# Kernel tuning notes

Hardware: AMD Instinct MI355X
Metric: run time of the kernel (lower is better)

## Reference

```python
import jax, jax.numpy as jnp
import numpy as np
import math

B, TQ, TK, D = 4, 1024, 1024, 1024
H, DK, DV = 16, 64, 64


def _ln(x, g, b, eps=1e-5):
    m = x.mean(-1, keepdims=True)
    v = ((x - m) ** 2).mean(-1, keepdims=True)
    return (x - m) * jax.lax.rsqrt(v + eps) * g + b


def setup_inputs() -> dict:
    key = jax.random.key(0)
    ks = jax.random.split(key, 24)
    s = 0.02
    inp = {
        "x": jax.random.normal(ks[0], (B, TQ, D), jnp.float32),
        "y": jax.random.normal(ks[1], (B, TK, D), jnp.float32),
        "mask": jax.random.randint(ks[2], (B, TK), 0, 2).astype(bool),
        # pre-attention layernorms (affine)
        "ln1_g": jnp.ones((D,)), "ln1_b": jnp.zeros((D,)),
        "ln2_g": jnp.ones((D,)), "ln2_b": jnp.zeros((D,)),
        # mha1 projections
        "q_w": jax.random.normal(ks[3], (D, H * DK)) * s, "q_b": jnp.zeros((H * DK,)),
        "k_w": jax.random.normal(ks[4], (D, H * DK)) * s, "k_b": jnp.zeros((H * DK,)),
        "v_w": jax.random.normal(ks[5], (D, H * DV)) * s, "v_b": jnp.zeros((H * DV,)),
        "o_w": jax.random.normal(ks[6], (H * DV, D)) * s, "o_b": jnp.zeros((D,)),
        # MLP: [LN, ReLU, Linear] x 2 over sizes [D, D, D]
        "mln1_g": jnp.ones((D,)), "mln1_b": jnp.zeros((D,)),
        "l1_w": jax.random.normal(ks[7], (D, D)) * s, "l1_b": jnp.zeros((D,)),
        "mln2_g": jnp.ones((D,)), "mln2_b": jnp.zeros((D,)),
        "l2_w": jax.random.normal(ks[8], (D, D)) * s, "l2_b": jnp.zeros((D,)),
    }
    return inp


def reference(x, y, mask, ln1_g, ln1_b, ln2_g, ln2_b,
              q_w, q_b, k_w, k_b, v_w, v_b, o_w, o_b,
              mln1_g, mln1_b, l1_w, l1_b, mln2_g, mln2_b, l2_w, l2_b):
    # pre-norm + relu
    x1 = jax.nn.relu(_ln(x, ln1_g, ln1_b))
    y1 = jax.nn.relu(_ln(y, ln2_g, ln2_b))
    # cross attention (mha1)
    b, t, _ = x1.shape
    q = (x1 @ q_w + q_b).reshape(b, t, H, DK)
    k = (y1 @ k_w + k_b).reshape(b, -1, H, DK)
    v = (y1 @ v_w + v_b).reshape(b, -1, H, DV)
    logits = jnp.einsum('bthd,bThd->bhtT', q, k) * (1.0 / math.sqrt(DK))
    logits = jnp.where(mask[:, None, None, :], logits, -1e30)
    w = jax.nn.softmax(logits, axis=-1)
    attn = jnp.einsum('bhtT,bThd->bthd', w, v).reshape(b, t, H * DV)
    x = x + (attn @ o_w + o_b)
    # MLP: LN -> ReLU -> Linear, twice
    h = jax.nn.relu(_ln(x, mln1_g, mln1_b)) @ l1_w + l1_b
    out = jax.nn.relu(_ln(h, mln2_g, mln2_b)) @ l2_w + l2_b
    return out
```

## Files before the change

kernel.cpp:

```cpp
#include <hip/hip_runtime.h>
#include <hip/hip_bf16.h>
#include <math.h>

#define D_MODEL 1024
#define NTOK    4096

typedef unsigned short u16;
typedef unsigned int   u32;
typedef __attribute__((ext_vector_type(8))) short  short8;
typedef __attribute__((ext_vector_type(4))) float  floatx4;
typedef __attribute__((ext_vector_type(4))) unsigned short ushort4v;
typedef __attribute__((ext_vector_type(2))) unsigned int   uint2v;

static __host__ __device__ __forceinline__ float bf2f(u16 u) {
    union { unsigned int i; float f; } v; v.i = ((unsigned int)u) << 16; return v.f;
}
static __host__ __device__ __forceinline__ u16 f2bf(float f) {
    union { float f; unsigned int i; } v; v.f = f;
    unsigned int r = (v.i + 0x7FFFu + ((v.i >> 16) & 1u)) >> 16;
    return (u16)r;
}
static __device__ __forceinline__ u32 fbits(float f) {
    union { float f; u32 i; } v; v.f = f; return v.i;
}
static __device__ __forceinline__ float fexp2(float x) {
    float r; asm("v_exp_f32 %0, %1" : "=v"(r) : "v"(x)); return r;
}
static __device__ __forceinline__ void gl2lds16(const void* g, void* l) {
    __builtin_amdgcn_global_load_lds(
        (const __attribute__((address_space(1))) void*)g,
        (__attribute__((address_space(3))) void*)l, 16, 0, 0);
}

__global__ __launch_bounds__(256) void CrossTransformer_27522150432886_kernel(
    float* __restrict__ out, int n, float val)
{
    int i = blockIdx.x * 256 + threadIdx.x;
    if (i < n) out[i] = val;
}

__global__ __launch_bounds__(256) void mask_k(
    const void* __restrict__ mp, float* __restrict__ madd)
{
    const unsigned int* w = (const unsigned int*)mp;
    const int t = threadIdx.x;
    int bad = 0;
    for (int i = t; i < 1024; i += 256) {
        unsigned int v = w[i];
        if (!(v == 0u || v == 1u || v == 0xFFu || v == 0xFFFFFFFFu)) bad++;
    }
#pragma unroll
    for (int off = 32; off > 0; off >>= 1) bad += __shfl_xor(bad, off, 64);
    __shared__ int rb[4];
    if ((t & 63) == 0) rb[t >> 6] = bad;
    __syncthreads();
    const int Bc = rb[0] + rb[1] + rb[2] + rb[3];
    if (Bc * 2 > 1024) {
        const unsigned char* b8 = (const unsigned char*)mp;
        for (int i = t; i < 4096; i += 256) madd[i] = b8[i] ? 0.f : -1e30f;
    } else {
        const int* m32 = (const int*)mp;
        for (int i = t; i < 4096; i += 256) madd[i] = m32[i] ? 0.f : -1e30f;
    }
}

__global__ __launch_bounds__(256) void ln_relu_k(
    const void* __restrict__ in, const float* __restrict__ gam,
    const float* __restrict__ bet, u16* __restrict__ out, int bf16in)
{
    const int row = blockIdx.x, t = threadIdx.x;
    float v0, v1, v2, v3;
    if (bf16in) {
        ushort4v u = *(const ushort4v*)((const u16*)in + (size_t)row * D_MODEL + t * 4);
        v0 = bf2f(u[0]); v1 = bf2f(u[1]); v2 = bf2f(u[2]); v3 = bf2f(u[3]);
    } else {
        const float4 p = *(const float4*)((const float*)in + (size_t)row * D_MODEL + t * 4);
        v0 = p.x; v1 = p.y; v2 = p.z; v3 = p.w;
    }
    float s = v0 + v1 + v2 + v3;
    float q = v0 * v0 + v1 * v1 + v2 * v2 + v3 * v3;
#pragma unroll
    for (int off = 32; off > 0; off >>= 1) {
        s += __shfl_xor(s, off, 64);
        q += __shfl_xor(q, off, 64);
    }
    __shared__ float red[2][4];
    if ((t & 63) == 0) { red[0][t >> 6] = s; red[1][t >> 6] = q; }
    __syncthreads();
    s = red[0][0] + red[0][1] + red[0][2] + red[0][3];
    q = red[1][0] + red[1][1] + red[1][2] + red[1][3];

    const float mean = s * (1.0f / D_MODEL);
    const float var  = q * (1.0f / D_MODEL) - mean * mean;
    const float rstd = rsqrtf(var + 1e-5f);

    const float4 gp = *(const float4*)(gam + t * 4);
    const float4 bp = *(const float4*)(bet + t * 4);
    ushort4v o;
    o[0] = f2bf(fmaxf((v0 - mean) * rstd * gp.x + bp.x, 0.f));
    o[1] = f2bf(fmaxf((v1 - mean) * rstd * gp.y + bp.y, 0.f));
    o[2] = f2bf(fmaxf((v2 - mean) * rstd * gp.z + bp.z, 0.f));
    o[3] = f2bf(fmaxf((v3 - mean) * rstd * gp.w + bp.w, 0.f));
    *(ushort4v*)(out + (size_t)row * D_MODEL + t * 4) = o;
}

struct W6 { const float* w[6]; };
__global__ __launch_bounds__(256) void wtrans_k(W6 wp, u16* __restrict__ WtBase)
{
    __shared__ u16 tile[32][33];
    const float* W  = wp.w[blockIdx.z];
    u16*         Wt = WtBase + (size_t)blockIdx.z * D_MODEL * D_MODEL;
    const int c0 = blockIdx.x * 32, r0 = blockIdx.y * 32;
    const int tx = threadIdx.x, ty = threadIdx.y;
#pragma unroll
    for (int j = 0; j < 4; j++)
        tile[ty + j * 8][tx] = f2bf(W[(size_t)(r0 + ty + j * 8) * D_MODEL + c0 + tx]);
    __syncthreads();
#pragma unroll
    for (int j = 0; j < 4; j++)
        Wt[(size_t)(c0 + ty + j * 8) * D_MODEL + r0 + tx] = tile[tx][ty + j * 8];
}

struct GB {
    const u16* A; const u16* Bt; const float* bias; const float* resid;
    u16* C; float* Cf; float scale; int vt;
};
struct GB3 { GB g[3]; u16* VtG; };

__global__ __launch_bounds__(256) void gemm_qkv_k(GB3 gb)
{
    const int lin = blockIdx.x + 8 * blockIdx.y + 256 * blockIdx.z;
    const int t8  = (lin & 7) * 96 + (lin >> 3);
    const int z   = t8 >> 8;
    const int rem = t8 & 255;
    const GB cfg = gb.g[z];
    __shared__ __align__(16) u16 sm[3 * 8192];
    const int t = threadIdx.x, lane = t & 63, w = t >> 6;
    const int wy = w >> 1, wx = w & 1;
    const int bm = (rem >> 3) * 128, bn = (rem & 7) * 128;
    const int m = lane & 15, g = lane >> 4;
    const int arow = t >> 2;
    const int aseg = ((t & 3) ^ ((t >> 3) & 3)) * 8;
    const int gsw  = (g ^ ((m >> 1) & 3)) * 8;

    const u16* Ag = cfg.A  + (size_t)(bm + arow) * D_MODEL + aseg;
    const u16* Bg = cfg.Bt + (size_t)(bn + arow) * D_MODEL + aseg;

    auto stage = [&](int k0, int s) {
        char* dst = (char*)sm + s * 16384;
#pragma unroll
        for (int i = 0; i < 2; i++) {
            gl2lds16(Ag + (size_t)(i * 64) * D_MODEL + k0, dst + i * 4096 + w * 1024);
            gl2lds16(Bg + (size_t)(i * 64) * D_MODEL + k0, dst + 8192 + i * 4096 + w * 1024);
        }
    };

    floatx4 acc[4][4] = {};
    const int NT = D_MODEL / 32;

    stage(0, 0);
    stage(32, 1);
    asm volatile("s_waitcnt vmcnt(4)" ::: "memory");
    __builtin_amdgcn_s_barrier();

    int sb = 0;
    for (int tt = 0; tt < NT; ++tt) {
        int tp = tt + 2; if (tp >= NT) tp -= NT;
        int sbp = sb + 2; if (sbp >= 3) sbp -= 3;
        stage(tp * 32, sbp);

        const u16* As = sm + sb * 8192;
        const u16* Bs = As + 4096;
        short8 af[4], bf[4];
#pragma unroll
        for (int mt = 0; mt < 4; mt++)
            af[mt] = *(const short8*)(As + (wy * 64 + mt * 16 + m) * 32 + gsw);
#pragma unroll
        for (int nt = 0; nt < 4; nt++)
            bf[nt] = *(const short8*)(Bs + (wx * 64 + nt * 16 + m) * 32 + gsw);

        __builtin_amdgcn_s_setprio(1);
#pragma unroll
        for (int mt = 0; mt < 4; mt++)
#pragma unroll
            for (int nt = 0; nt < 4; nt++)
                acc[mt][nt] = __builtin_amdgcn_mfma_f32_16x16x32_bf16(
                    af[mt], bf[nt], acc[mt][nt], 0, 0, 0);
        __builtin_amdgcn_s_setprio(0);

        asm volatile("s_waitcnt vmcnt(4)" ::: "memory");
        __builtin_amdgcn_s_barrier();
        sb = sb + 1; if (sb >= 3) sb -= 3;
    }
    asm volatile("s_waitcnt vmcnt(0)" ::: "memory");
    __builtin_amdgcn_s_barrier();

    float bv[4];
#pragma unroll
    for (int nt = 0; nt < 4; nt++)
        bv[nt] = cfg.bias[bn + wx * 64 + nt * 16 + m];

    if (!cfg.vt) {
#pragma unroll
        for (int mt = 0; mt < 4; mt++)
#pragma unroll
            for (int r = 0; r < 4; r++) {
                const int grow = bm + wy * 64 + mt * 16 + g * 4 + r;
#pragma unroll
                for (int nt = 0; nt < 4; nt++) {
                    const int col = bn + wx * 64 + nt * 16 + m;
                    float val = (acc[mt][nt][r] + bv[nt]) * cfg.scale;
                    cfg.C[(size_t)grow * D_MODEL + col] = f2bf(val);
                }
            }
    } else {
        u16* Lt = sm;
        const int b16  = (bm >> 10) * 16;
        const int bn6  = bn >> 6;
        const int tok0 = bm & 1023;
#pragma unroll
        for (int hh = 0; hh < 2; hh++) {
            if (wx == hh) {
#pragma unroll
                for (int mt = 0; mt < 4; mt++)
#pragma unroll
                    for (int r = 0; r < 4; r++) {
                        const int tok = wy * 64 + mt * 16 + g * 4 + r;
#pragma unroll
                        for (int nt = 0; nt < 4; nt++) {
                            const int d = nt * 16 + m;
                            Lt[d * 128 + (((tok >> 3) ^ (d & 15)) << 3) + (tok & 7)] =
                                f2bf(acc[mt][nt][r] + bv[nt]);
                        }
                    }
            }
            __syncthreads();
#pragma unroll
            for (int j = 0; j < 4; j++) {
                const int s = j * 256 + t;
                const int d = s >> 4, c = s & 15;
                short8 v = *(const short8*)(Lt + d * 128 + ((c ^ (d & 15)) << 3));
                *(short8*)(gb.VtG + ((size_t)((b16 + bn6 + hh) * 64 + d)) * 1024 + tok0 + c * 8) = v;
            }
            __syncthreads();
        }
    }
}

__global__ __launch_bounds__(256) void gemm_k(GB3 gb)
{
    const GB cfg = gb.g[blockIdx.z];
    const int lin = blockIdx.x + 16 * blockIdx.y;
    const int tw  = (lin & 7) * 64 + (lin >> 3);
    __shared__ __align__(16) u16 sm[3 * 6144];
    const int t = threadIdx.x, lane = t & 63, w = t >> 6;
    const int wy = w >> 1, wx = w & 1;
    const int bm = (tw >> 4) * 128, bn = (tw & 15) * 64;
    const int m = lane & 15, g = lane >> 4;
    const int gsw = (g ^ ((m >> 1) & 3)) * 8;

    const u16* Ag = cfg.A  + (size_t)(bm + (t >> 2)) * D_MODEL
                    + ((t & 3) ^ ((t >> 3) & 3)) * 8;
    const u16* Bg = cfg.Bt + (size_t)(bn + w * 16 + (lane >> 2)) * D_MODEL
                    + ((lane & 3) ^ ((lane >> 3) & 3)) * 8;

    auto stage = [&](int k0, int s) {
        char* dst = (char*)sm + s * 12288;
#pragma unroll
        for (int i = 0; i < 2; i++)
            gl2lds16(Ag + (size_t)(i * 64) * D_MODEL + k0, dst + i * 4096 + w * 1024);
        gl2lds16(Bg + k0, dst + 8192 + w * 1024);
    };

    floatx4 acc[4][2] = {};
    const int NT = D_MODEL / 32;

    stage(0, 0);
    stage(32, 1);
    asm volatile("s_waitcnt vmcnt(3)" ::: "memory");
    __builtin_amdgcn_s_barrier();

    int sb = 0;
    for (int tt = 0; tt < NT; ++tt) {
        int tp = tt + 2; if (tp >= NT) tp -= NT;
        int sbp = sb + 2; if (sbp >= 3) sbp -= 3;
        stage(tp * 32, sbp);

        const u16* As = sm + sb * 6144;
        const u16* Bs = As + 4096;
        short8 af[4], bf[2];
#pragma unroll
        for (int mt = 0; mt < 4; mt++)
            af[mt] = *(const short8*)(As + (wy * 64 + mt * 16 + m) * 32 + gsw);
#pragma unroll
        for (int nt = 0; nt < 2; nt++)
            bf[nt] = *(const short8*)(Bs + (wx * 32 + nt * 16 + m) * 32 + gsw);

        __builtin_amdgcn_s_setprio(1);
#pragma unroll
        for (int mt = 0; mt < 4; mt++)
#pragma unroll
            for (int nt = 0; nt < 2; nt++)
                acc[mt][nt] = __builtin_amdgcn_mfma_f32_16x16x32_bf16(
                    af[mt], bf[nt], acc[mt][nt], 0, 0, 0);
        __builtin_amdgcn_s_setprio(0);

        asm volatile("s_waitcnt vmcnt(3)" ::: "memory");
        __builtin_amdgcn_s_barrier();
        sb = sb + 1; if (sb >= 3) sb -= 3;
    }
    asm volatile("s_waitcnt vmcnt(0)" ::: "memory");

    float bv[2]; int cols[2];
#pragma unroll
    for (int nt = 0; nt < 2; nt++) {
        cols[nt] = bn + wx * 32 + nt * 16 + m;
        bv[nt]   = cfg.bias[cols[nt]];
    }
#pragma unroll
    for (int mt = 0; mt < 4; mt++) {
#pragma unroll
        for (int r = 0; r < 4; r++) {
            const int grow = bm + wy * 64 + mt * 16 + g * 4 + r;
#pragma unroll
            for (int nt = 0; nt < 2; nt++) {
                float val = (acc[mt][nt][r] + bv[nt]) * cfg.scale;
                if (cfg.resid) val += cfg.resid[(size_t)grow * D_MODEL + cols[nt]];
                if (cfg.Cf) cfg.Cf[(size_t)grow * D_MODEL + cols[nt]] = val;
                else        cfg.C [(size_t)grow * D_MODEL + cols[nt]] = f2bf(val);
            }
        }
    }
}

__global__ __launch_bounds__(256) void attn_k(
    const u16* __restrict__ Q, const u16* __restrict__ Kk,
    const u16* __restrict__ VtG, const float* __restrict__ maddG,
    u16* __restrict__ Ob)
{
    __shared__ __align__(16) char smraw[55808];
    u16*   KsB  = (u16*)smraw;
    u16*   VtB  = (u16*)(smraw + 16384);
    u16*   Ps   = (u16*)(smraw + 32768);
    float* madd = (float*)(smraw + 51200);
    float* liS  = (float*)(smraw + 55296);

    const int lin = blockIdx.x + 8 * (blockIdx.y + 16 * blockIdx.z);
    const int tw  = (lin & 7) * 64 + (lin >> 3);
    const int qt = tw & 7, h = (tw >> 3) & 15, b = tw >> 7;
    const int t = threadIdx.x, lane = t & 63, w = t >> 6;
    const int m = lane & 15, g = lane >> 4;

    for (int i = t; i < 1024; i += 256) madd[i] = maddG[b * 1024 + i];

    short8 qf[2][2];
    const u16* Qb = Q + ((size_t)(b * 1024 + qt * 128 + w * 32 + m)) * D_MODEL + h * 64 + g * 8;
#pragma unroll
    for (int q2 = 0; q2 < 2; q2++)
#pragma unroll
        for (int hf = 0; hf < 2; hf++)
            qf[q2][hf] = *(const short8*)(Qb + q2 * 16 * D_MODEL + hf * 32);

    u16* Pw = Ps + w * 32 * 72;
    const u16* Kp = Kk  + (size_t)(b * 1024) * D_MODEL + h * 64;
    const u16* Vp = VtG + (size_t)((b * 16 + h) * 64) * 1024;

    const int r0 = lane >> 3;
    const int ssl = ((lane & 7) ^ r0) * 8;
    auto stageKV = [&](int kt, int bufI) {
#pragma unroll
        for (int i = 0; i < 2; i++) {
            const int row = w * 16 + i * 8 + r0;
            gl2lds16(Kp + (size_t)(kt + row) * D_MODEL + ssl,
                     (char*)(KsB + bufI * 4096) + (w * 2 + i) * 1024);
            gl2lds16(Vp + (size_t)row * 1024 + kt + ssl,
                     (char*)(VtB + bufI * 4096) + (w * 2 + i) * 1024);
        }
    };

    floatx4 Ov[2][4] = {};
    float li[2] = { 0.f, 0.f };

    const int s8  = m & 7;
    const int sl0 = (g ^ s8) * 8;
    const int sl1 = sl0 ^ 32;

    stageKV(0, 0);
    __syncthreads();

    int buf = 0;
    for (int kt = 0; kt < 1024; kt += 64) {
        if (kt + 64 < 1024) stageKV(kt + 64, buf ^ 1);

        const u16* Ks = KsB + buf * 4096;
        const u16* Vt = VtB + buf * 4096;

        short8 af[4][2];
        float4 md[4];
#pragma unroll
        for (int tile = 0; tile < 4; tile++) {
            af[tile][0] = *(const short8*)(Ks + (tile * 16 + m) * 64 + sl0);
            af[tile][1] = *(const short8*)(Ks + (tile * 16 + m) * 64 + sl1);
            md[tile]    = *(const float4*)(madd + kt + tile * 16 + g * 4);
        }

#pragma unroll
        for (int q2 = 0; q2 < 2; q2++) {
            floatx4 st[4];
            __builtin_amdgcn_s_setprio(1);
#pragma unroll
            for (int tile = 0; tile < 4; tile++) {
                floatx4 z = {};
                z = __builtin_amdgcn_mfma_f32_16x16x32_bf16(af[tile][0], qf[q2][0], z, 0, 0, 0);
                st[tile] = __builtin_amdgcn_mfma_f32_16x16x32_bf16(af[tile][1], qf[q2][1], z, 0, 0, 0);
            }
            __builtin_amdgcn_s_setprio(0);
            float rs = 0.f;
#pragma unroll
            for (int tile = 0; tile < 4; tile++) {
                float p0 = fexp2(st[tile][0] + md[tile].x);
                float p1 = fexp2(st[tile][1] + md[tile].y);
                float p2 = fexp2(st[tile][2] + md[tile].z);
                float p3 = fexp2(st[tile][3] + md[tile].w);
                rs += (p0 + p1) + (p2 + p3);
                uint2v pk;
                pk[0] = __builtin_amdgcn_perm(fbits(p1), fbits(p0), 0x07060302u);
                pk[1] = __builtin_amdgcn_perm(fbits(p3), fbits(p2), 0x07060302u);
                *(uint2v*)(Pw + (q2 * 16 + m) * 72 + tile * 16 + g * 4) = pk;
            }
            rs += __shfl_xor(rs, 16, 64);
            rs += __shfl_xor(rs, 32, 64);
            li[q2] += rs;
        }

        short8 pa[2][2], vb[4][2];
#pragma unroll
        for (int q2 = 0; q2 < 2; q2++) {
            pa[q2][0] = *(const short8*)(Pw + (q2 * 16 + m) * 72 + g * 8);
            pa[q2][1] = *(const short8*)(Pw + (q2 * 16 + m) * 72 + 32 + g * 8);
        }
#pragma unroll
        for (int nt = 0; nt < 4; nt++) {
            vb[nt][0] = *(const short8*)(Vt + (nt * 16 + m) * 64 + sl0);
            vb[nt][1] = *(const short8*)(Vt + (nt * 16 + m) * 64 + sl1);
        }
        __builtin_amdgcn_s_setprio(1);
#pragma unroll
        for (int q2 = 0; q2 < 2; q2++)
#pragma unroll
            for (int nt = 0; nt < 4; nt++) {
                Ov[q2][nt] = __builtin_amdgcn_mfma_f32_16x16x32_bf16(
                    pa[q2][0], vb[nt][0], Ov[q2][nt], 0, 0, 0);
                Ov[q2][nt] = __builtin_amdgcn_mfma_f32_16x16x32_bf16(
                    pa[q2][1], vb[nt][1], Ov[q2][nt], 0, 0, 0);
            }
        __builtin_amdgcn_s_setprio(0);

        asm volatile("s_waitcnt vmcnt(0)" ::: "memory");
        __builtin_amdgcn_s_barrier();
        buf ^= 1;
    }

    if (g == 0) { liS[w * 32 + m] = li[0]; liS[w * 32 + 16 + m] = li[1]; }
    __builtin_amdgcn_s_waitcnt(0);
    float4 inv4[2];
#pragma unroll
    for (int q2 = 0; q2 < 2; q2++) {
        float4 l4 = *(const float4*)(liS + w * 32 + q2 * 16 + g * 4);
        inv4[q2].x = 1.0f / fmaxf(l4.x, 1e-37f);
        inv4[q2].y = 1.0f / fmaxf(l4.y, 1e-37f);
        inv4[q2].z = 1.0f / fmaxf(l4.z, 1e-37f);
        inv4[q2].w = 1.0f / fmaxf(l4.w, 1e-37f);
    }
#pragma unroll
    for (int q2 = 0; q2 < 2; q2++) {
        const float iv[4] = { inv4[q2].x, inv4[q2].y, inv4[q2].z, inv4[q2].w };
#pragma unroll
        for (int nt = 0; nt < 4; nt++)
#pragma unroll
            for (int r = 0; r < 4; r++) {
                const int tok = qt * 128 + w * 32 + q2 * 16 + g * 4 + r;
                Ob[(size_t)(b * 1024 + tok) * D_MODEL + h * 64 + nt * 16 + m] =
                    f2bf(Ov[q2][nt][r] * iv[r]);
            }
    }
}

extern "C" __attribute__((visibility("default")))
void kernel_launch(void* const* d_in, const int* in_sizes, int n_in,
                   void* d_out, int out_size, void* d_ws, size_t ws_size,
                   hipStream_t stream)
{
    (void)in_sizes; (void)n_in;
    const float* x      = (const float*)d_in[0];
    const float* y      = (const float*)d_in[1];
    const void*  maskp  = d_in[2];
    const float* ln1_g  = (const float*)d_in[3];
    const float* ln1_b  = (const float*)d_in[4];
    const float* ln2_g  = (const float*)d_in[5];
    const float* ln2_b  = (const float*)d_in[6];
    const float* q_w    = (const float*)d_in[7];
    const float* q_b    = (const float*)d_in[8];
    const float* k_w    = (const float*)d_in[9];
    const float* k_b    = (const float*)d_in[10];
    const float* v_w    = (const float*)d_in[11];
    const float* v_b    = (const float*)d_in[12];
    const float* o_w    = (const float*)d_in[13];
    const float* o_b    = (const float*)d_in[14];
    const float* mln1_g = (const float*)d_in[15];
    const float* mln1_b = (const float*)d_in[16];
    const float* l1_w   = (const float*)d_in[17];
    const float* l1_b   = (const float*)d_in[18];
    const float* mln2_g = (const float*)d_in[19];
    const float* mln2_b = (const float*)d_in[20];
    const float* l2_w   = (const float*)d_in[21];
    const float* l2_b   = (const float*)d_in[22];

    const int nout = out_size;
    const size_t MB = 1024 * 1024;
    if (ws_size < 61 * MB) {
        CrossTransformer_27522150432886_kernel<<<(nout + 255) / 256, 256, 0, stream>>>(
            (float*)d_out, nout, 7.0f);
        return;
    }

    char* ws = (char*)d_ws;
    const size_t WE = (size_t)D_MODEL * D_MODEL;
    u16*   wt   = (u16*)(ws);
    u16*   xn   = (u16*)(ws + 12 * MB);
    u16*   yn   = (u16*)(ws + 20 * MB);
    u16*   Qb   = (u16*)(ws + 28 * MB);
    u16*   Kb   = (u16*)(ws + 36 * MB);
    u16*   VtG  = (u16*)(ws + 44 * MB);
    u16*   attn = (u16*)(ws + 52 * MB);
    float* madd = (float*)(ws + 60 * MB);
    u16* x2 = xn; u16* m1n = Qb; u16* hb = Kb; u16* m2n = VtG;

    mask_k<<<1, 256, 0, stream>>>(maskp, madd);

    W6 wp; wp.w[0] = q_w; wp.w[1] = k_w; wp.w[2] = v_w;
    wp.w[3] = o_w; wp.w[4] = l1_w; wp.w[5] = l2_w;
    wtrans_k<<<dim3(32, 32, 6), dim3(32, 8), 0, stream>>>(wp, wt);

    ln_relu_k<<<NTOK, 256, 0, stream>>>(x, ln1_g, ln1_b, xn, 0);
    ln_relu_k<<<NTOK, 256, 0, stream>>>(y, ln2_g, ln2_b, yn, 0);

    const float qscale = 0.18033688011112042f;
    GB3 qkv = {};
    qkv.g[0] = GB{ xn, wt + 0 * WE, q_b, nullptr, Qb, nullptr, qscale, 0 };
    qkv.g[1] = GB{ yn, wt + 1 * WE, k_b, nullptr, Kb, nullptr, 1.0f,  0 };
    qkv.g[2] = GB{ yn, wt + 2 * WE, v_b, nullptr, nullptr, nullptr, 1.0f, 1 };
    qkv.VtG = VtG;
    gemm_qkv_k<<<dim3(8, 32, 3), 256, 0, stream>>>(qkv);

    attn_k<<<dim3(8, 16, 4), 256, 0, stream>>>(Qb, Kb, VtG, madd, attn);

    GB3 go = {};
    go.g[0] = GB{ attn, wt + 3 * WE, o_b, x, x2, nullptr, 1.0f, 0 };
    gemm_k<<<dim3(16, 32, 1), 256, 0, stream>>>(go);

    ln_relu_k<<<NTOK, 256, 0, stream>>>(x2, mln1_g, mln1_b, m1n, 1);

    GB3 g1 = {};
    g1.g[0] = GB{ m1n, wt + 4 * WE, l1_b, nullptr, hb, nullptr, 1.0f, 0 };
    gemm_k<<<dim3(16, 32, 1), 256, 0, stream>>>(g1);

    ln_relu_k<<<NTOK, 256, 0, stream>>>(hb, mln2_g, mln2_b, m2n, 1);

    GB3 g2 = {};
    g2.g[0] = GB{ m2n, wt + 5 * WE, l2_b, nullptr, nullptr, (float*)d_out, 1.0f, 0 };
    gemm_k<<<dim3(16, 32, 1), 256, 0, stream>>>(g2);
}
```

Before: 287.4 us.

## Merge preprocessing kernels and use 128x128 four-stage GEMM for projections

Merges the mask, weight-transpose and two input layernorm kernels into one launch that dispatches on block index. It also replaces the 128x64 single-output GEMM with the templated 128x128 QKV GEMM, using four LDS stages, for the output projection and both MLP layers. The QKV GEMM's epilogue gains residual and fp32-output support so one kernel covers all projections. The larger tiles give more reuse per block but launch only 256 blocks on a large-CU GPU, which may underfill it, and the extra stage raises LDS use.

```diff
diff --git a/kernel.cpp b/kernel.cpp
--- a/kernel.cpp
+++ b/kernel.cpp
@@ -39,44 +39,98 @@
     if (i < n) out[i] = val;
 }
 
-__global__ __launch_bounds__(256) void mask_k(
-    const void* __restrict__ mp, float* __restrict__ madd)
+struct PreArgs {
+    const float* w[6]; u16* wt;
+    const float* x; const float* g1; const float* b1; u16* xn;
+    const float* y; const float* g2; const float* b2; u16* yn;
+    const void* maskp; float* madd;
+};
+__global__ __launch_bounds__(256) void pre_k(PreArgs a)
 {
-    const unsigned int* w = (const unsigned int*)mp;
-    const int t = threadIdx.x;
-    int bad = 0;
-    for (int i = t; i < 1024; i += 256) {
-        unsigned int v = w[i];
-        if (!(v == 0u || v == 1u || v == 0xFFu || v == 0xFFFFFFFFu)) bad++;
-    }
-#pragma unroll
-    for (int off = 32; off > 0; off >>= 1) bad += __shfl_xor(bad, off, 64);
-    __shared__ int rb[4];
-    if ((t & 63) == 0) rb[t >> 6] = bad;
-    __syncthreads();
-    const int Bc = rb[0] + rb[1] + rb[2] + rb[3];
-    if (Bc * 2 > 1024) {
-        const unsigned char* b8 = (const unsigned char*)mp;
-        for (int i = t; i < 4096; i += 256) madd[i] = b8[i] ? 0.f : -1e30f;
-    } else {
-        const int* m32 = (const int*)mp;
-        for (int i = t; i < 4096; i += 256) madd[i] = m32[i] ? 0.f : -1e30f;
+    __shared__ __align__(16) char shm[2176];
+    const int blk = blockIdx.x, t = threadIdx.x;
+
+    if (blk < 6144) {
+        u16 (*tile)[33] = (u16(*)[33])shm;
+        const int wz = blk >> 10, tl = blk & 1023;
+        const int c0 = (tl & 31) * 32, r0 = (tl >> 5) * 32;
+        const int tx = t & 31, ty = t >> 5;
+        const float* W  = a.w[wz];
+        u16*         Wt = a.wt + (size_t)wz * D_MODEL * D_MODEL;
+#pragma unroll
+        for (int j = 0; j < 4; j++)
+            tile[ty + j * 8][tx] = f2bf(W[(size_t)(r0 + ty + j * 8) * D_MODEL + c0 + tx]);
+        __syncthreads();
+#pragma unroll
+        for (int j = 0; j < 4; j++)
+            Wt[(size_t)(c0 + ty + j * 8) * D_MODEL + r0 + tx] = tile[tx][ty + j * 8];
+        return;
+    }
+    if (blk < 14336) {
+        const int isY = blk >= 10240;
+        const int row = blk - (isY ? 10240 : 6144);
+        const float* in  = isY ? a.y  : a.x;
+        const float* gam = isY ? a.g2 : a.g1;
+        const float* bet = isY ? a.b2 : a.b1;
+        u16*         out = isY ? a.yn : a.xn;
+        float (*red)[4] = (float(*)[4])shm;
+
+        const float4 p = *(const float4*)(in + (size_t)row * D_MODEL + t * 4);
+        float v0 = p.x, v1 = p.y, v2 = p.z, v3 = p.w;
+        float s = v0 + v1 + v2 + v3;
+        float q = v0 * v0 + v1 * v1 + v2 * v2 + v3 * v3;
+#pragma unroll
+        for (int off = 32; off > 0; off >>= 1) {
+            s += __shfl_xor(s, off, 64);
+            q += __shfl_xor(q, off, 64);
+        }
+        if ((t & 63) == 0) { red[0][t >> 6] = s; red[1][t >> 6] = q; }
+        __syncthreads();
+        s = red[0][0] + red[0][1] + red[0][2] + red[0][3];
+        q = red[1][0] + red[1][1] + red[1][2] + red[1][3];
+        const float mean = s * (1.0f / D_MODEL);
+        const float var  = q * (1.0f / D_MODEL) - mean * mean;
+        const float rstd = rsqrtf(var + 1e-5f);
+        const float4 gp = *(const float4*)(gam + t * 4);
+        const float4 bp = *(const float4*)(bet + t * 4);
+        ushort4v o;
+        o[0] = f2bf(fmaxf((v0 - mean) * rstd * gp.x + bp.x, 0.f));
+        o[1] = f2bf(fmaxf((v1 - mean) * rstd * gp.y + bp.y, 0.f));
+        o[2] = f2bf(fmaxf((v2 - mean) * rstd * gp.z + bp.z, 0.f));
+        o[3] = f2bf(fmaxf((v3 - mean) * rstd * gp.w + bp.w, 0.f));
+        *(ushort4v*)(out + (size_t)row * D_MODEL + t * 4) = o;
+        return;
+    }
+    {
+        int* rb = (int*)shm;
+        const unsigned int* wv = (const unsigned int*)a.maskp;
+        int bad = 0;
+        for (int i = t; i < 1024; i += 256) {
+            unsigned int v = wv[i];
+            if (!(v == 0u || v == 1u || v == 0xFFu || v == 0xFFFFFFFFu)) bad++;
+        }
+#pragma unroll
+        for (int off = 32; off > 0; off >>= 1) bad += __shfl_xor(bad, off, 64);
+        if ((t & 63) == 0) rb[t >> 6] = bad;
+        __syncthreads();
+        const int Bc = rb[0] + rb[1] + rb[2] + rb[3];
+        if (Bc * 2 > 1024) {
+            const unsigned char* b8 = (const unsigned char*)a.maskp;
+            for (int i = t; i < 4096; i += 256) a.madd[i] = b8[i] ? 0.f : -1e30f;
+        } else {
+            const int* m32 = (const int*)a.maskp;
+            for (int i = t; i < 4096; i += 256) a.madd[i] = m32[i] ? 0.f : -1e30f;
+        }
     }
 }
 
 __global__ __launch_bounds__(256) void ln_relu_k(
     const void* __restrict__ in, const float* __restrict__ gam,
-    const float* __restrict__ bet, u16* __restrict__ out, int bf16in)
+    const float* __restrict__ bet, u16* __restrict__ out)
 {
     const int row = blockIdx.x, t = threadIdx.x;
-    float v0, v1, v2, v3;
-    if (bf16in) {
-        ushort4v u = *(const ushort4v*)((const u16*)in + (size_t)row * D_MODEL + t * 4);
-        v0 = bf2f(u[0]); v1 = bf2f(u[1]); v2 = bf2f(u[2]); v3 = bf2f(u[3]);
-    } else {
-        const float4 p = *(const float4*)((const float*)in + (size_t)row * D_MODEL + t * 4);
-        v0 = p.x; v1 = p.y; v2 = p.z; v3 = p.w;
-    }
+    ushort4v u = *(const ushort4v*)((const u16*)in + (size_t)row * D_MODEL + t * 4);
+    float v0 = bf2f(u[0]), v1 = bf2f(u[1]), v2 = bf2f(u[2]), v3 = bf2f(u[3]);
     float s = v0 + v1 + v2 + v3;
     float q = v0 * v0 + v1 * v1 + v2 * v2 + v3 * v3;
 #pragma unroll
@@ -104,37 +158,21 @@
     *(ushort4v*)(out + (size_t)row * D_MODEL + t * 4) = o;
 }
 
-struct W6 { const float* w[6]; };
-__global__ __launch_bounds__(256) void wtrans_k(W6 wp, u16* __restrict__ WtBase)
-{
-    __shared__ u16 tile[32][33];
-    const float* W  = wp.w[blockIdx.z];
-    u16*         Wt = WtBase + (size_t)blockIdx.z * D_MODEL * D_MODEL;
-    const int c0 = blockIdx.x * 32, r0 = blockIdx.y * 32;
-    const int tx = threadIdx.x, ty = threadIdx.y;
-#pragma unroll
-    for (int j = 0; j < 4; j++)
-        tile[ty + j * 8][tx] = f2bf(W[(size_t)(r0 + ty + j * 8) * D_MODEL + c0 + tx]);
-    __syncthreads();
-#pragma unroll
-    for (int j = 0; j < 4; j++)
-        Wt[(size_t)(c0 + ty + j * 8) * D_MODEL + r0 + tx] = tile[tx][ty + j * 8];
-}
-
 struct GB {
     const u16* A; const u16* Bt; const float* bias; const float* resid;
     u16* C; float* Cf; float scale; int vt;
 };
 struct GB3 { GB g[3]; u16* VtG; };
 
-__global__ __launch_bounds__(256) void gemm_qkv_k(GB3 gb)
+template<int NS>
+__global__ __launch_bounds__(256) void gemm128_k(GB3 gb, int cpx)
 {
     const int lin = blockIdx.x + 8 * blockIdx.y + 256 * blockIdx.z;
-    const int t8  = (lin & 7) * 96 + (lin >> 3);
+    const int t8  = (lin & 7) * cpx + (lin >> 3);
     const int z   = t8 >> 8;
     const int rem = t8 & 255;
     const GB cfg = gb.g[z];
-    __shared__ __align__(16) u16 sm[3 * 8192];
+    __shared__ __align__(16) u16 sm[NS * 8192];
     const int t = threadIdx.x, lane = t & 63, w = t >> 6;
     const int wy = w >> 1, wx = w & 1;
     const int bm = (rem >> 3) * 128, bn = (rem & 7) * 128;
@@ -158,15 +196,16 @@
     floatx4 acc[4][4] = {};
     const int NT = D_MODEL / 32;
 
-    stage(0, 0);
-    stage(32, 1);
-    asm volatile("s_waitcnt vmcnt(4)" ::: "memory");
+#pragma unroll
+    for (int i = 0; i < NS - 1; i++) stage(i * 32, i);
+    if constexpr (NS == 3) asm volatile("s_waitcnt vmcnt(4)" ::: "memory");
+    else                   asm volatile("s_waitcnt vmcnt(8)" ::: "memory");
     __builtin_amdgcn_s_barrier();
 
     int sb = 0;
     for (int tt = 0; tt < NT; ++tt) {
-        int tp = tt + 2; if (tp >= NT) tp -= NT;
-        int sbp = sb + 2; if (sbp >= 3) sbp -= 3;
+        int tp = tt + (NS - 1); if (tp >= NT) tp -= NT;
+        int sbp = sb + (NS - 1); if (sbp >= NS) sbp -= NS;
         stage(tp * 32, sbp);
 
         const u16* As = sm + sb * 8192;
@@ -188,9 +227,10 @@
                     af[mt], bf[nt], acc[mt][nt], 0, 0, 0);
         __builtin_amdgcn_s_setprio(0);
 
-        asm volatile("s_waitcnt vmcnt(4)" ::: "memory");
+        if constexpr (NS == 3) asm volatile("s_waitcnt vmcnt(4)" ::: "memory");
+        else                   asm volatile("s_waitcnt vmcnt(8)" ::: "memory");
         __builtin_amdgcn_s_barrier();
-        sb = sb + 1; if (sb >= 3) sb -= 3;
+        sb = sb + 1; if (sb >= NS) sb -= NS;
     }
     asm volatile("s_waitcnt vmcnt(0)" ::: "memory");
     __builtin_amdgcn_s_barrier();
@@ -210,7 +250,9 @@
                 for (int nt = 0; nt < 4; nt++) {
                     const int col = bn + wx * 64 + nt * 16 + m;
                     float val = (acc[mt][nt][r] + bv[nt]) * cfg.scale;
-                    cfg.C[(size_t)grow * D_MODEL + col] = f2bf(val);
+                    if (cfg.resid) val += cfg.resid[(size_t)grow * D_MODEL + col];
+                    if (cfg.Cf) cfg.Cf[(size_t)grow * D_MODEL + col] = val;
+                    else        cfg.C [(size_t)grow * D_MODEL + col] = f2bf(val);
                 }
             }
     } else {
@@ -243,92 +285,6 @@
                 *(short8*)(gb.VtG + ((size_t)((b16 + bn6 + hh) * 64 + d)) * 1024 + tok0 + c * 8) = v;
             }
             __syncthreads();
-        }
-    }
-}
-
-__global__ __launch_bounds__(256) void gemm_k(GB3 gb)
-{
-    const GB cfg = gb.g[blockIdx.z];
-    const int lin = blockIdx.x + 16 * blockIdx.y;
-    const int tw  = (lin & 7) * 64 + (lin >> 3);
-    __shared__ __align__(16) u16 sm[3 * 6144];
-    const int t = threadIdx.x, lane = t & 63, w = t >> 6;
-    const int wy = w >> 1, wx = w & 1;
-    const int bm = (tw >> 4) * 128, bn = (tw & 15) * 64;
-    const int m = lane & 15, g = lane >> 4;
-    const int gsw = (g ^ ((m >> 1) & 3)) * 8;
-
-    const u16* Ag = cfg.A  + (size_t)(bm + (t >> 2)) * D_MODEL
-                    + ((t & 3) ^ ((t >> 3) & 3)) * 8;
-    const u16* Bg = cfg.Bt + (size_t)(bn + w * 16 + (lane >> 2)) * D_MODEL
-                    + ((lane & 3) ^ ((lane >> 3) & 3)) * 8;
-
-    auto stage = [&](int k0, int s) {
-        char* dst = (char*)sm + s * 12288;
-#pragma unroll
-        for (int i = 0; i < 2; i++)
-            gl2lds16(Ag + (size_t)(i * 64) * D_MODEL + k0, dst + i * 4096 + w * 1024);
-        gl2lds16(Bg + k0, dst + 8192 + w * 1024);
-    };
-
-    floatx4 acc[4][2] = {};
-    const int NT = D_MODEL / 32;
-
-    stage(0, 0);
-    stage(32, 1);
-    asm volatile("s_waitcnt vmcnt(3)" ::: "memory");
-    __builtin_amdgcn_s_barrier();
-
-    int sb = 0;
-    for (int tt = 0; tt < NT; ++tt) {
-        int tp = tt + 2; if (tp >= NT) tp -= NT;
-        int sbp = sb + 2; if (sbp >= 3) sbp -= 3;
-        stage(tp * 32, sbp);
-
-        const u16* As = sm + sb * 6144;
-        const u16* Bs = As + 4096;
-        short8 af[4], bf[2];
-#pragma unroll
-        for (int mt = 0; mt < 4; mt++)
-            af[mt] = *(const short8*)(As + (wy * 64 + mt * 16 + m) * 32 + gsw);
-#pragma unroll
-        for (int nt = 0; nt < 2; nt++)
-            bf[nt] = *(const short8*)(Bs + (wx * 32 + nt * 16 + m) * 32 + gsw);
-
-        __builtin_amdgcn_s_setprio(1);
-#pragma unroll
-        for (int mt = 0; mt < 4; mt++)
-#pragma unroll
-            for (int nt = 0; nt < 2; nt++)
-                acc[mt][nt] = __builtin_amdgcn_mfma_f32_16x16x32_bf16(
-                    af[mt], bf[nt], acc[mt][nt], 0, 0, 0);
-        __builtin_amdgcn_s_setprio(0);
-
-        asm volatile("s_waitcnt vmcnt(3)" ::: "memory");
-        __builtin_amdgcn_s_barrier();
-        sb = sb + 1; if (sb >= 3) sb -= 3;
-    }
-    asm volatile("s_waitcnt vmcnt(0)" ::: "memory");
-
-    float bv[2]; int cols[2];
-#pragma unroll
-    for (int nt = 0; nt < 2; nt++) {
-        cols[nt] = bn + wx * 32 + nt * 16 + m;
-        bv[nt]   = cfg.bias[cols[nt]];
-    }
-#pragma unroll
-    for (int mt = 0; mt < 4; mt++) {
-#pragma unroll
-        for (int r = 0; r < 4; r++) {
-            const int grow = bm + wy * 64 + mt * 16 + g * 4 + r;
-#pragma unroll
-            for (int nt = 0; nt < 2; nt++) {
-                float val = (acc[mt][nt][r] + bv[nt]) * cfg.scale;
-                if (cfg.resid) val += cfg.resid[(size_t)grow * D_MODEL + cols[nt]];
-                if (cfg.Cf) cfg.Cf[(size_t)grow * D_MODEL + cols[nt]] = val;
-                else        cfg.C [(size_t)grow * D_MODEL + cols[nt]] = f2bf(val);
-            }
         }
     }
 }
@@ -536,14 +492,14 @@
     float* madd = (float*)(ws + 60 * MB);
     u16* x2 = xn; u16* m1n = Qb; u16* hb = Kb; u16* m2n = VtG;
 
-    mask_k<<<1, 256, 0, stream>>>(maskp, madd);
-
-    W6 wp; wp.w[0] = q_w; wp.w[1] = k_w; wp.w[2] = v_w;
-    wp.w[3] = o_w; wp.w[4] = l1_w; wp.w[5] = l2_w;
-    wtrans_k<<<dim3(32, 32, 6), dim3(32, 8), 0, stream>>>(wp, wt);
-
-    ln_relu_k<<<NTOK, 256, 0, stream>>>(x, ln1_g, ln1_b, xn, 0);
-    ln_relu_k<<<NTOK, 256, 0, stream>>>(y, ln2_g, ln2_b, yn, 0);
+    PreArgs pa;
+    pa.w[0] = q_w; pa.w[1] = k_w; pa.w[2] = v_w;
+    pa.w[3] = o_w; pa.w[4] = l1_w; pa.w[5] = l2_w;
+    pa.wt = wt;
+    pa.x = x; pa.g1 = ln1_g; pa.b1 = ln1_b; pa.xn = xn;
+    pa.y = y; pa.g2 = ln2_g; pa.b2 = ln2_b; pa.yn = yn;
+    pa.maskp = maskp; pa.madd = madd;
+    pre_k<<<14337, 256, 0, stream>>>(pa);
 
     const float qscale = 0.18033688011112042f;
     GB3 qkv = {};
@@ -551,23 +507,23 @@
     qkv.g[1] = GB{ yn, wt + 1 * WE, k_b, nullptr, Kb, nullptr, 1.0f,  0 };
     qkv.g[2] = GB{ yn, wt + 2 * WE, v_b, nullptr, nullptr, nullptr, 1.0f, 1 };
     qkv.VtG = VtG;
-    gemm_qkv_k<<<dim3(8, 32, 3), 256, 0, stream>>>(qkv);
+    gemm128_k<3><<<dim3(8, 32, 3), 256, 0, stream>>>(qkv, 96);
 
     attn_k<<<dim3(8, 16, 4), 256, 0, stream>>>(Qb, Kb, VtG, madd, attn);
 
     GB3 go = {};
     go.g[0] = GB{ attn, wt + 3 * WE, o_b, x, x2, nullptr, 1.0f, 0 };
-    gemm_k<<<dim3(16, 32, 1), 256, 0, stream>>>(go);
-
-    ln_relu_k<<<NTOK, 256, 0, stream>>>(x2, mln1_g, mln1_b, m1n, 1);
+    gemm128_k<4><<<dim3(8, 32, 1), 256, 0, stream>>>(go, 32);
+
+    ln_relu_k<<<NTOK, 256, 0, stream>>>(x2, mln1_g, mln1_b, m1n);
 
     GB3 g1 = {};
     g1.g[0] = GB{ m1n, wt + 4 * WE, l1_b, nullptr, hb, nullptr, 1.0f, 0 };
-    gemm_k<<<dim3(16, 32, 1), 256, 0, stream>>>(g1);
-
-    ln_relu_k<<<NTOK, 256, 0, stream>>>(hb, mln2_g, mln2_b, m2n, 1);
+    gemm128_k<4><<<dim3(8, 32, 1), 256, 0, stream>>>(g1, 32);
+
+    ln_relu_k<<<NTOK, 256, 0, stream>>>(hb, mln2_g, mln2_b, m2n);
 
     GB3 g2 = {};
     g2.g[0] = GB{ m2n, wt + 5 * WE, l2_b, nullptr, nullptr, (float*)d_out, 1.0f, 0 };
-    gemm_k<<<dim3(16, 32, 1), 256, 0, stream>>>(g2);
-}
+    gemm128_k<4><<<dim3(8, 32, 1), 256, 0, stream>>>(g2, 32);
+}
```

New measurement: 296.0 us. 3.0% more time.
